# Kernel optimization log

Hardware: AMD Instinct MI355X
Metric: run time of the kernel (lower is better)

Reference implementation:

```python
import jax, jax.numpy as jnp
import numpy as np

B, N, E = 4, 10000, 160000
IN, HEADS, C = 128, 4, 64  # hidden_dim=64, num_heads=4 -> per-layer out = 256
OUT = HEADS * C
NEG_SLOPE = 0.2  # PyG GATConv default leaky_relu slope


def setup_inputs() -> dict:
    key = jax.random.key(0)
    ks = jax.random.split(key, 10)
    x = jax.random.normal(ks[0], (B, N, IN), dtype=jnp.float32)
    edge_index = jax.random.randint(ks[1], (2, E), 0, N, dtype=jnp.int64)
    s = 0.05
    W1 = jax.random.normal(ks[2], (IN, OUT), dtype=jnp.float32) * s
    a_src1 = jax.random.normal(ks[3], (HEADS, C), dtype=jnp.float32) * s
    a_dst1 = jax.random.normal(ks[4], (HEADS, C), dtype=jnp.float32) * s
    b1 = jnp.zeros((OUT,), dtype=jnp.float32)
    W2 = jax.random.normal(ks[5], (OUT, OUT), dtype=jnp.float32) * s
    a_src2 = jax.random.normal(ks[6], (HEADS, C), dtype=jnp.float32) * s
    a_dst2 = jax.random.normal(ks[7], (HEADS, C), dtype=jnp.float32) * s
    b2 = jnp.zeros((OUT,), dtype=jnp.float32)
    return {"x": x, "edge_index": edge_index,
            "W1": W1, "a_src1": a_src1, "a_dst1": a_dst1, "b1": b1,
            "W2": W2, "a_src2": a_src2, "a_dst2": a_dst2, "b2": b2}


def _gat_layer(h, W, a_src, a_dst, b, src, dst, n_nodes):
    # h: [N, in_dim]; src/dst: [E'] (self-loops included)
    hW = (h @ W).reshape(n_nodes, HEADS, C)            # [N, H, C]
    al_src = jnp.sum(hW * a_src, axis=-1)              # [N, H]
    al_dst = jnp.sum(hW * a_dst, axis=-1)              # [N, H]
    e = jax.nn.leaky_relu(al_src[src] + al_dst[dst], NEG_SLOPE)  # [E', H]
    # segment softmax over edges grouped by destination node
    m = jax.ops.segment_max(e, dst, num_segments=n_nodes)        # [N, H]
    ex = jnp.exp(e - m[dst])                                     # [E', H]
    denom = jax.ops.segment_sum(ex, dst, num_segments=n_nodes)   # [N, H]
    alpha = ex / (denom[dst] + 1e-16)                            # [E', H]
    out = jax.ops.segment_sum(alpha[:, :, None] * hW[src], dst, num_segments=n_nodes)  # [N, H, C]
    return out.reshape(n_nodes, OUT) + b


def reference(x, edge_index, W1, a_src1, a_dst1, b1, W2, a_src2, a_dst2, b2):
    n_nodes = x.shape[1]
    loops = jnp.arange(n_nodes, dtype=edge_index.dtype)
    src = jnp.concatenate([edge_index[0], loops])  # PyG GATConv adds self-loops
    dst = jnp.concatenate([edge_index[1], loops])

    def per_graph(xb):
        h = jax.nn.elu(_gat_layer(xb, W1, a_src1, a_dst1, b1, src, dst, n_nodes))
        h = jax.nn.elu(_gat_layer(h, W2, a_src2, a_dst2, b2, src, dst, n_nodes))
        return h  # dropout is identity in eval mode

    return jax.vmap(per_graph)(x)  # [B, N, OUT]
```

## Files before the change

kernel.cpp:

```cpp
#include <hip/hip_runtime.h>
#include <hip/hip_fp16.h>
#include <math.h>

#define NNODES 10000
#define NB 4
#define NIN 128
#define NOUT 256
#define NHEADS 4
#define NE 160000
#define NEP (NE + NNODES)
#define NEG_SLOPE 0.2f
#define MTOT (NB * NNODES)
#define MPAD 40064
#define DCAP 120

typedef _Float16 f16;
typedef f16 f16x4 __attribute__((ext_vector_type(4)));
typedef f16 f16x8 __attribute__((ext_vector_type(8)));
typedef float f32x4 __attribute__((ext_vector_type(4)));

typedef __attribute__((address_space(1))) const void* gas_p;
typedef __attribute__((address_space(3))) void* las_p;

__device__ __forceinline__ float lrelu(float x) { return x >= 0.f ? x : NEG_SLOPE * x; }

__device__ __forceinline__ __half2 h2shfl_xor(__half2 v, int off) {
  union { __half2 h; int i; } u;
  u.h = v;
  u.i = __shfl_xor(u.i, off, 64);
  return u.h;
}


__global__ void hist_kernel(const int* __restrict__ ei, int* __restrict__ deg) {
  int e = blockIdx.x * blockDim.x + threadIdx.x;
  if (e >= NEP) return;
  int d = (e < NE) ? ei[NE + e] : (e - NE);
  atomicAdd(&deg[d], 1);
}

__global__ __launch_bounds__(1024) void scan_kernel(const int* __restrict__ deg,
                                                    int* __restrict__ offs,
                                                    int* __restrict__ cursor) {
  __shared__ int buf[1024];
  const int t = threadIdx.x;
  const int base = t * 10;
  int loc[10];
  int tot = 0;
  #pragma unroll
  for (int j = 0; j < 10; ++j) {
    int i = base + j;
    int v = (i < NNODES) ? deg[i] : 0;
    tot += v;
    loc[j] = tot;
  }
  buf[t] = tot;
  __syncthreads();
  #pragma unroll
  for (int off = 1; off < 1024; off <<= 1) {
    int v = (t >= off) ? buf[t - off] : 0;
    __syncthreads();
    buf[t] += v;
    __syncthreads();
  }
  const int excl = buf[t] - tot;
  #pragma unroll
  for (int j = 0; j < 10; ++j) {
    int i = base + j;
    if (i < NNODES) {
      int o = excl + (j ? loc[j - 1] : 0);
      offs[i] = o;
      cursor[i] = o;
    }
  }
  if (t == 1023) offs[NNODES] = buf[1023];
}

__global__ void scatter_kernel(const int* __restrict__ ei, int* __restrict__ cursor,
                               int* __restrict__ csr) {
  int e = blockIdx.x * blockDim.x + threadIdx.x;
  if (e >= NEP) return;
  int s, d;
  if (e < NE) { s = ei[e]; d = ei[NE + e]; } else { s = e - NE; d = s; }
  int pos = atomicAdd(&cursor[d], 1);
  csr[pos] = s;
}


#define NXV (MTOT * NIN / 4)

__global__ void cvt_all_kernel(const float* __restrict__ x,
                               const float* __restrict__ W1,
                               const float* __restrict__ W2,
                               f16* __restrict__ x16,
                               f16* __restrict__ W1t,
                               f16* __restrict__ W2t) {
  int i = blockIdx.x * blockDim.x + threadIdx.x;
  if (i < NXV) {
    float4 v = ((const float4*)x)[i];
    f16x4 o = {(f16)v.x, (f16)v.y, (f16)v.z, (f16)v.w};
    *((f16x4*)x16 + i) = o;
    return;
  }
  i -= NXV;
  if (i < NIN * NOUT) {
    int k = i >> 8, c = i & 255;
    W1t[c * NIN + k] = (f16)W1[i];
    return;
  }
  i -= NIN * NOUT;
  if (i < NOUT * NOUT) {
    int k = i >> 8, c = i & 255;
    W2t[c * NOUT + k] = (f16)W2[i];
  }
}


template<int K>
__global__ __launch_bounds__(256) void mfma_gemm(const f16* __restrict__ A,
                                                 const f16* __restrict__ Bt,
                                                 f16* __restrict__ C,
                                                 const float* __restrict__ a_src,
                                                 const float* __restrict__ a_dst,
                                                 float* __restrict__ alS,
                                                 float* __restrict__ alD) {
  __shared__ f16 As[128 * 32];
  __shared__ f16 Bs[128 * 32];
  const int tid  = threadIdx.x;
  const int lane = tid & 63;
  const int wid  = tid >> 6;
  const int bm = blockIdx.x * 128;
  const int bn = blockIdx.y * 128;
  const int wr = (wid >> 1) * 64;
  const int wc = (wid & 1) * 64;
  f32x4 acc[4][4] = {};

  const int srow   = lane >> 2;
  const int schnk0 = lane & 3;

  for (int k0 = 0; k0 < K; k0 += 32) {
    #pragma unroll
    for (int t = 0; t < 2; ++t) {
      int rb  = wid * 32 + t * 16;
      int row = rb + srow;
      int sc  = schnk0 ^ ((row >> 1) & 3);
      __builtin_amdgcn_global_load_lds((gas_p)(A  + (size_t)(bm + row) * K + k0 + sc * 8),
                                       (las_p)(As + rb * 32), 16, 0, 0);
      __builtin_amdgcn_global_load_lds((gas_p)(Bt + (size_t)(bn + row) * K + k0 + sc * 8),
                                       (las_p)(Bs + rb * 32), 16, 0, 0);
    }
    __syncthreads();

    f16x8 av[4], bv[4];
    const int fr = lane & 15;
    const int kc = lane >> 4;
    #pragma unroll
    for (int i = 0; i < 4; ++i) {
      int ra = wr + i * 16 + fr;
      av[i] = *(const f16x8*)(As + ra * 32 + ((kc ^ ((ra >> 1) & 3)) * 8));
      int rb2 = wc + i * 16 + fr;
      bv[i] = *(const f16x8*)(Bs + rb2 * 32 + ((kc ^ ((rb2 >> 1) & 3)) * 8));
    }
    #pragma unroll
    for (int i = 0; i < 4; ++i)
      #pragma unroll
      for (int j = 0; j < 4; ++j)
        acc[i][j] = __builtin_amdgcn_mfma_f32_16x16x32_f16(av[i], bv[j], acc[i][j], 0, 0, 0);
    __syncthreads();
  }

  const int fr = lane & 15;
  const int rg = lane >> 4;
  #pragma unroll
  for (int i = 0; i < 4; ++i)
    #pragma unroll
    for (int r = 0; r < 4; ++r) {
      size_t row = bm + wr + i * 16 + rg * 4 + r;
      #pragma unroll
      for (int j = 0; j < 4; ++j) {
        int col = bn + wc + j * 16 + fr;
        C[row * NOUT + col] = (f16)acc[i][j][r];
      }
    }

  const int hb = (bn + wc) >> 6;
  float aS[4], aD[4];
  #pragma unroll
  for (int j = 0; j < 4; ++j) {
    int c = hb * 64 + j * 16 + fr;
    aS[j] = a_src[c];
    aD[j] = a_dst[c];
  }
  float sS[4][4], sD[4][4];
  #pragma unroll
  for (int i = 0; i < 4; ++i)
    #pragma unroll
    for (int r = 0; r < 4; ++r) {
      float vS = 0.f, vD = 0.f;
      #pragma unroll
      for (int j = 0; j < 4; ++j) {
        vS = fmaf(acc[i][j][r], aS[j], vS);
        vD = fmaf(acc[i][j][r], aD[j], vD);
      }
      sS[i][r] = vS;
      sD[i][r] = vD;
    }
  #pragma unroll
  for (int off = 1; off < 16; off <<= 1)
    #pragma unroll
    for (int i = 0; i < 4; ++i)
      #pragma unroll
      for (int r = 0; r < 4; ++r) {
        sS[i][r] += __shfl_xor(sS[i][r], off, 64);
        sD[i][r] += __shfl_xor(sD[i][r], off, 64);
      }
  if (fr == 0) {
    #pragma unroll
    for (int i = 0; i < 4; ++i)
      #pragma unroll
      for (int r = 0; r < 4; ++r) {
        size_t row = bm + wr + i * 16 + rg * 4 + r;
        if (row < MTOT) {
          alS[row * 4 + hb] = sS[i][r];
          alD[row * 4 + hb] = sD[i][r];
        }
      }
  }
}


template<bool F16OUT>
__global__ __launch_bounds__(256) void gat_edge_kernel(
    const f16* __restrict__ hW, const float* __restrict__ alS,
    const float* __restrict__ alD, const int* __restrict__ offs,
    const int* __restrict__ csr, const float* __restrict__ bias,
    float* __restrict__ outF, f16* __restrict__ outH) {
  __shared__ float e_lds[4][DCAP][4];
  __shared__ int   u_lds[4][DCAP];
  __shared__ float lds[4][256];
  const int bid  = blockIdx.x;
  const int xcd  = bid & 7;
  const int b    = xcd >> 1;
  const int l    = (bid >> 3) * 2 + (xcd & 1);
  const int slot = (int)threadIdx.x >> 6;
  const int node = l * 4 + slot;
  const int lane = (int)threadIdx.x & 63;

  const f16*   hWb  = hW  + (size_t)b * NNODES * NOUT;
  const float* alSb = alS + (size_t)b * NNODES * NHEADS;
  const float* alDb = alD + (size_t)b * NNODES * NHEADS;
  const int beg = offs[node];
  const int end = offs[node + 1];

  const int h1 = lane & 3;
  const int es = lane >> 2;
  const float ald1 = alDb[node * 4 + h1];
  float m = -1e30f, s = 0.f;
  for (int i = beg + es; i < end; i += 16) {
    int u = csr[i];
    float e = lrelu(alSb[u * 4 + h1] + ald1);
    int idx = i - beg;
    if (idx < DCAP) {
      e_lds[slot][idx][h1] = e;
      if (h1 == 0) u_lds[slot][idx] = u;
    }
    float mn = fmaxf(m, e);
    s = s * __expf(m - mn) + __expf(e - mn);
    m = mn;
  }
  #pragma unroll
  for (int off = 4; off < 64; off <<= 1) {
    float mo = __shfl_xor(m, off, 64);
    float so = __shfl_xor(s, off, 64);
    float mn = fmaxf(m, mo);
    s = s * __expf(m - mn) + so * __expf(mo - mn);
    m = mn;
  }
  float m4[4], i4[4], d4[4];
  #pragma unroll
  for (int h = 0; h < 4; ++h) {
    m4[h] = __shfl(m, h, 64);
    float sh = __shfl(s, h, 64);
    i4[h] = 1.0f / (sh + 1e-16f);
    d4[h] = __shfl(ald1, h, 64);
  }

  const int k3  = lane >> 3;
  const int sub = lane & 7;
  __half2 acc2[16];
  #pragma unroll
  for (int q = 0; q < 16; ++q) acc2[q] = __float2half2_rn(0.f);

  for (int i = beg + k3; i < end; i += 8) {
    int idx = i - beg;
    int u;
    float4 ev;
    if (idx < DCAP) {
      u = u_lds[slot][idx];
      ev = *(const float4*)&e_lds[slot][idx][0];
    } else {
      u = csr[i];
      float4 als = *(const float4*)(alSb + (size_t)u * 4);
      ev = make_float4(lrelu(als.x + d4[0]), lrelu(als.y + d4[1]),
                       lrelu(als.z + d4[2]), lrelu(als.w + d4[3]));
    }
    __half2 a2[4];
    a2[0] = __float2half2_rn(__expf(ev.x - m4[0]) * i4[0]);
    a2[1] = __float2half2_rn(__expf(ev.y - m4[1]) * i4[1]);
    a2[2] = __float2half2_rn(__expf(ev.z - m4[2]) * i4[2]);
    a2[3] = __float2half2_rn(__expf(ev.w - m4[3]) * i4[3]);
    const __half2* hp = (const __half2*)(hWb + (size_t)u * NOUT);
    #pragma unroll
    for (int q = 0; q < 4; ++q) {
      const __half2* cp = hp + (q * 8 + sub) * 4;
      #pragma unroll
      for (int p = 0; p < 4; ++p)
        acc2[q * 4 + p] = __hfma2(a2[q], cp[p], acc2[q * 4 + p]);
    }
  }

  #pragma unroll
  for (int off = 8; off < 64; off <<= 1)
    #pragma unroll
    for (int q = 0; q < 16; ++q)
      acc2[q] = __hadd2(acc2[q], h2shfl_xor(acc2[q], off));

  if (k3 == 0) {
    #pragma unroll
    for (int q = 0; q < 4; ++q)
      #pragma unroll
      for (int p = 0; p < 4; ++p) {
        float2 f = __half22float2(acc2[q * 4 + p]);
        int ch = (q * 8 + sub) * 8 + p * 2;
        lds[slot][ch]     = f.x;
        lds[slot][ch + 1] = f.y;
      }
  }
  __syncthreads();

  float4 r = *(const float4*)&lds[slot][lane * 4];
  float4 bb = *(const float4*)(bias + lane * 4);
  r.x += bb.x; r.y += bb.y; r.z += bb.z; r.w += bb.w;
  r.x = r.x > 0.f ? r.x : (__expf(r.x) - 1.f);
  r.y = r.y > 0.f ? r.y : (__expf(r.y) - 1.f);
  r.z = r.z > 0.f ? r.z : (__expf(r.z) - 1.f);
  r.w = r.w > 0.f ? r.w : (__expf(r.w) - 1.f);

  const size_t o = ((size_t)b * NNODES + node) * NOUT + lane * 4;
  if (F16OUT) {
    f16x4 hv = {(f16)r.x, (f16)r.y, (f16)r.z, (f16)r.w};
    *(f16x4*)(outH + o) = hv;
  } else {
    *(float4*)(outF + o) = r;
  }
}


extern "C" void kernel_launch(void* const* d_in, const int* in_sizes, int n_in,
                              void* d_out, int out_size, void* d_ws, size_t ws_size,
                              hipStream_t stream) {
  const float* x   = (const float*)d_in[0];
  const int*   ei  = (const int*)d_in[1];
  const float* W1  = (const float*)d_in[2];
  const float* as1 = (const float*)d_in[3];
  const float* ad1 = (const float*)d_in[4];
  const float* b1  = (const float*)d_in[5];
  const float* W2  = (const float*)d_in[6];
  const float* as2 = (const float*)d_in[7];
  const float* ad2 = (const float*)d_in[8];
  const float* b2  = (const float*)d_in[9];
  float* out = (float*)d_out;

  char* p = (char*)d_ws;
  auto carve = [&](size_t bytes) -> void* {
    void* q = (void*)p;
    p += (bytes + 255) & ~(size_t)255;
    return q;
  };
  int*   deg    = (int*)carve((size_t)NNODES * 4);
  int*   offs   = (int*)carve((size_t)(NNODES + 1) * 4);
  int*   cursor = (int*)carve((size_t)NNODES * 4);
  int*   csr    = (int*)carve((size_t)NEP * 4);
  f16*   hW16   = (f16*)carve((size_t)MPAD * NOUT * 2);
  float* alS    = (float*)carve((size_t)MTOT * NHEADS * 4);
  float* alD    = (float*)carve((size_t)MTOT * NHEADS * 4);
  f16*   W1t    = (f16*)carve((size_t)NOUT * NIN * 2);
  f16*   W2t    = (f16*)carve((size_t)NOUT * NOUT * 2);

  f16* x16 = (f16*)d_out;
  f16* h1  = (f16*)((char*)d_out + (size_t)MPAD * NIN * 2);

  hipMemsetAsync(deg, 0, (size_t)NNODES * 4, stream);
  hist_kernel<<<(NEP + 255) / 256, 256, 0, stream>>>(ei, deg);
  scan_kernel<<<1, 1024, 0, stream>>>(deg, offs, cursor);
  scatter_kernel<<<(NEP + 255) / 256, 256, 0, stream>>>(ei, cursor, csr);

  const int cvt_items = NXV + NIN * NOUT + NOUT * NOUT;
  cvt_all_kernel<<<(cvt_items + 255) / 256, 256, 0, stream>>>(x, W1, W2, x16, W1t, W2t);

  dim3 ggrid(MPAD / 128, NOUT / 128);

  mfma_gemm<NIN><<<ggrid, 256, 0, stream>>>(x16, W1t, hW16, as1, ad1, alS, alD);
  gat_edge_kernel<true><<<NNODES, 256, 0, stream>>>(hW16, alS, alD, offs, csr, b1, nullptr, h1);

  mfma_gemm<NOUT><<<ggrid, 256, 0, stream>>>(h1, W2t, hW16, as2, ad2, alS, alD);
  gat_edge_kernel<false><<<NNODES, 256, 0, stream>>>(hW16, alS, alD, offs, csr, b2, out, nullptr);
}
```

Measured before the change: 255.6 us.

## Drop max-subtraction in edge softmax, reshape edge lanes, fuse histogram into convert

The edge kernel no longer tracks a running max for the softmax. It stores exp(min(e,60)) in LDS and sums plain exponentials, which removes the online-max rescaling and the max reduction. The aggregation loop now processes 4 edges at a time with 16 lanes per edge, each lane covering 16 channels of one head, so fewer cross-lane reductions are needed. The degree histogram is fused into the convert kernel to save a launch, and DCAP drops to 64. Omitting max subtraction risks overflow or lost precision for large logits, which the clamp at 60 only partly guards against.

```diff
diff --git a/kernel.cpp b/kernel.cpp
--- a/kernel.cpp
+++ b/kernel.cpp
@@ -12,7 +12,7 @@
 #define NEG_SLOPE 0.2f
 #define MTOT (NB * NNODES)
 #define MPAD 40064
-#define DCAP 120
+#define DCAP 64
 
 typedef _Float16 f16;
 typedef f16 f16x4 __attribute__((ext_vector_type(4)));
@@ -31,13 +31,6 @@
   return u.h;
 }
 
-
-__global__ void hist_kernel(const int* __restrict__ ei, int* __restrict__ deg) {
-  int e = blockIdx.x * blockDim.x + threadIdx.x;
-  if (e >= NEP) return;
-  int d = (e < NE) ? ei[NE + e] : (e - NE);
-  atomicAdd(&deg[d], 1);
-}
 
 __global__ __launch_bounds__(1024) void scan_kernel(const int* __restrict__ deg,
                                                     int* __restrict__ offs,
@@ -88,14 +81,22 @@
 
 
 #define NXV (MTOT * NIN / 4)
-
-__global__ void cvt_all_kernel(const float* __restrict__ x,
-                               const float* __restrict__ W1,
-                               const float* __restrict__ W2,
-                               f16* __restrict__ x16,
-                               f16* __restrict__ W1t,
-                               f16* __restrict__ W2t) {
-  int i = blockIdx.x * blockDim.x + threadIdx.x;
+#define CVT_ITEMS (NXV + NIN * NOUT + NOUT * NOUT)
+
+__global__ void cvt_hist_kernel(const float* __restrict__ x,
+                                const float* __restrict__ W1,
+                                const float* __restrict__ W2,
+                                const int* __restrict__ ei,
+                                f16* __restrict__ x16,
+                                f16* __restrict__ W1t,
+                                f16* __restrict__ W2t,
+                                int* __restrict__ deg) {
+  int t = blockIdx.x * blockDim.x + threadIdx.x;
+  if (t < NEP) {
+    int d = (t < NE) ? ei[NE + t] : (t - NE);
+    atomicAdd(&deg[d], 1);
+  }
+  int i = t;
   if (i < NXV) {
     float4 v = ((const float4*)x)[i];
     f16x4 o = {(f16)v.x, (f16)v.y, (f16)v.z, (f16)v.w};
@@ -235,7 +236,7 @@
     const float* __restrict__ alD, const int* __restrict__ offs,
     const int* __restrict__ csr, const float* __restrict__ bias,
     float* __restrict__ outF, f16* __restrict__ outH) {
-  __shared__ float e_lds[4][DCAP][4];
+  __shared__ float p_lds[4][DCAP][4];
   __shared__ int   u_lds[4][DCAP];
   __shared__ float lds[4][256];
   const int bid  = blockIdx.x;
@@ -255,86 +256,62 @@
   const int h1 = lane & 3;
   const int es = lane >> 2;
   const float ald1 = alDb[node * 4 + h1];
-  float m = -1e30f, s = 0.f;
+  float s = 0.f;
   for (int i = beg + es; i < end; i += 16) {
     int u = csr[i];
     float e = lrelu(alSb[u * 4 + h1] + ald1);
+    float pp = __expf(fminf(e, 60.f));
     int idx = i - beg;
     if (idx < DCAP) {
-      e_lds[slot][idx][h1] = e;
+      p_lds[slot][idx][h1] = pp;
       if (h1 == 0) u_lds[slot][idx] = u;
     }
-    float mn = fmaxf(m, e);
-    s = s * __expf(m - mn) + __expf(e - mn);
-    m = mn;
-  }
-  #pragma unroll
-  for (int off = 4; off < 64; off <<= 1) {
-    float mo = __shfl_xor(m, off, 64);
-    float so = __shfl_xor(s, off, 64);
-    float mn = fmaxf(m, mo);
-    s = s * __expf(m - mn) + so * __expf(mo - mn);
-    m = mn;
-  }
-  float m4[4], i4[4], d4[4];
-  #pragma unroll
-  for (int h = 0; h < 4; ++h) {
-    m4[h] = __shfl(m, h, 64);
-    float sh = __shfl(s, h, 64);
-    i4[h] = 1.0f / (sh + 1e-16f);
-    d4[h] = __shfl(ald1, h, 64);
-  }
-
-  const int k3  = lane >> 3;
-  const int sub = lane & 7;
-  __half2 acc2[16];
-  #pragma unroll
-  for (int q = 0; q < 16; ++q) acc2[q] = __float2half2_rn(0.f);
-
-  for (int i = beg + k3; i < end; i += 8) {
+    s += pp;
+  }
+  #pragma unroll
+  for (int off = 4; off < 64; off <<= 1) s += __shfl_xor(s, off, 64);
+
+  const int k3  = lane >> 4;
+  const int sub = lane & 15;
+  const int hh  = sub >> 2;
+  const float inv = 1.0f / (__shfl(s, hh, 64) + 1e-16f);
+  const float dh  = __shfl(ald1, hh, 64);
+
+  __half2 acc2[8];
+  #pragma unroll
+  for (int q = 0; q < 8; ++q) acc2[q] = __float2half2_rn(0.f);
+
+  for (int i = beg + k3; i < end; i += 4) {
     int idx = i - beg;
     int u;
-    float4 ev;
+    float pp;
     if (idx < DCAP) {
-      u = u_lds[slot][idx];
-      ev = *(const float4*)&e_lds[slot][idx][0];
+      u  = u_lds[slot][idx];
+      pp = p_lds[slot][idx][hh];
     } else {
-      u = csr[i];
-      float4 als = *(const float4*)(alSb + (size_t)u * 4);
-      ev = make_float4(lrelu(als.x + d4[0]), lrelu(als.y + d4[1]),
-                       lrelu(als.z + d4[2]), lrelu(als.w + d4[3]));
-    }
-    __half2 a2[4];
-    a2[0] = __float2half2_rn(__expf(ev.x - m4[0]) * i4[0]);
-    a2[1] = __float2half2_rn(__expf(ev.y - m4[1]) * i4[1]);
-    a2[2] = __float2half2_rn(__expf(ev.z - m4[2]) * i4[2]);
-    a2[3] = __float2half2_rn(__expf(ev.w - m4[3]) * i4[3]);
-    const __half2* hp = (const __half2*)(hWb + (size_t)u * NOUT);
-    #pragma unroll
-    for (int q = 0; q < 4; ++q) {
-      const __half2* cp = hp + (q * 8 + sub) * 4;
-      #pragma unroll
-      for (int p = 0; p < 4; ++p)
-        acc2[q * 4 + p] = __hfma2(a2[q], cp[p], acc2[q * 4 + p]);
-    }
-  }
-
-  #pragma unroll
-  for (int off = 8; off < 64; off <<= 1)
-    #pragma unroll
-    for (int q = 0; q < 16; ++q)
+      u  = csr[i];
+      pp = __expf(fminf(lrelu(alSb[u * 4 + hh] + dh), 60.f));
+    }
+    __half2 a2 = __float2half2_rn(pp * inv);
+    const __half2* cp = (const __half2*)(hWb + (size_t)u * NOUT + sub * 16);
+    #pragma unroll
+    for (int q = 0; q < 8; ++q)
+      acc2[q] = __hfma2(a2, cp[q], acc2[q]);
+  }
+
+  #pragma unroll
+  for (int off = 16; off < 64; off <<= 1)
+    #pragma unroll
+    for (int q = 0; q < 8; ++q)
       acc2[q] = __hadd2(acc2[q], h2shfl_xor(acc2[q], off));
 
   if (k3 == 0) {
     #pragma unroll
-    for (int q = 0; q < 4; ++q)
-      #pragma unroll
-      for (int p = 0; p < 4; ++p) {
-        float2 f = __half22float2(acc2[q * 4 + p]);
-        int ch = (q * 8 + sub) * 8 + p * 2;
-        lds[slot][ch]     = f.x;
-        lds[slot][ch + 1] = f.y;
-      }
+    for (int q = 0; q < 8; ++q) {
+      float2 f = __half22float2(acc2[q]);
+      lds[slot][sub * 16 + q * 2]     = f.x;
+      lds[slot][sub * 16 + q * 2 + 1] = f.y;
+    }
   }
   __syncthreads();
 
@@ -391,13 +368,11 @@
   f16* h1  = (f16*)((char*)d_out + (size_t)MPAD * NIN * 2);
 
   hipMemsetAsync(deg, 0, (size_t)NNODES * 4, stream);
-  hist_kernel<<<(NEP + 255) / 256, 256, 0, stream>>>(ei, deg);
+  cvt_hist_kernel<<<(CVT_ITEMS + 255) / 256, 256, 0, stream>>>(x, W1, W2, ei,
+                                                               x16, W1t, W2t, deg);
   scan_kernel<<<1, 1024, 0, stream>>>(deg, offs, cursor);
   scatter_kernel<<<(NEP + 255) / 256, 256, 0, stream>>>(ei, cursor, csr);
 
-  const int cvt_items = NXV + NIN * NOUT + NOUT * NOUT;
-  cvt_all_kernel<<<(cvt_items + 255) / 256, 256, 0, stream>>>(x, W1, W2, x16, W1t, W2t);
-
   dim3 ggrid(MPAD / 128, NOUT / 128);
 
   mfma_gemm<NIN><<<ggrid, 256, 0, stream>>>(x16, W1t, hW16, as1, ad1, alS, alD);
```

Measured after the change: 235.7 us. 7.8% less time.
